# Optimization experiments

Hardware: AMD Instinct MI355X
Metric: run time of the kernel (lower is better)

## Reference

```python
import jax, jax.numpy as jnp
import numpy as np

V, SMAX, D, L, H, F = 50257, 1024, 768, 12, 12, 3072
DH = D // H
SCALE = float(np.sqrt(DH))


def setup_inputs() -> dict:
    key = jax.random.key(0)
    ks = jax.random.split(key, 24)
    B, S = 2, 1024
    std = 0.02
    inp = {
        'input_ids': jax.random.randint(ks[0], (B, S), 0, V),
        'tok_emb': jax.random.normal(ks[1], (V, D), jnp.float32) * std,
        'pos_emb': jax.random.normal(ks[2], (SMAX, D), jnp.float32) * std,
        # stacked per-layer params (leading dim L)
        'Wq': jax.random.normal(ks[3], (L, D, D), jnp.float32) * std,
        'bq': jnp.zeros((L, D), jnp.float32),
        'Wk': jax.random.normal(ks[4], (L, D, D), jnp.float32) * std,
        'bk': jnp.zeros((L, D), jnp.float32),
        'Wv': jax.random.normal(ks[5], (L, D, D), jnp.float32) * std,
        'bv': jnp.zeros((L, D), jnp.float32),
        'Wo': jax.random.normal(ks[6], (L, D, D), jnp.float32) * std,
        'bo': jnp.zeros((L, D), jnp.float32),
        'ln1_g': jnp.ones((L, D), jnp.float32),
        'ln1_b': jnp.zeros((L, D), jnp.float32),
        'ln2_g': jnp.ones((L, D), jnp.float32),
        'ln2_b': jnp.zeros((L, D), jnp.float32),
        'W1': jax.random.normal(ks[7], (L, D, F), jnp.float32) * std,
        'b1': jnp.zeros((L, F), jnp.float32),
        'W2': jax.random.normal(ks[8], (L, F, D), jnp.float32) * std,
        'b2': jnp.zeros((L, D), jnp.float32),
        'lnf_g': jnp.ones((D,), jnp.float32),
        'lnf_b': jnp.zeros((D,), jnp.float32),
        'Whead': jax.random.normal(ks[9], (D, V), jnp.float32) * std,
    }
    return inp


def _layernorm(x, g, b, eps=1e-5):
    mu = jnp.mean(x, axis=-1, keepdims=True)
    var = jnp.var(x, axis=-1, keepdims=True)
    return (x - mu) * jax.lax.rsqrt(var + eps) * g + b


def _gpt_forward(input_ids, tok_emb, pos_emb, Wq, bq, Wk, bk, Wv, bv, Wo, bo,
                 ln1_g, ln1_b, ln2_g, ln2_b, W1, b1, W2, b2, lnf_g, lnf_b, Whead):
    B, S = input_ids.shape
    x = tok_emb[input_ids] + pos_emb[:S][None, :, :]  # (B,S,D)
    # additive causal mask: -inf above the diagonal
    idx = jnp.arange(S)
    neg_inf = jnp.finfo(x.dtype).min
    mask = jnp.where(idx[None, :] > idx[:, None], neg_inf, 0.0).astype(x.dtype)  # (S,S)

    def block(x, p):
        (wq, bq_, wk, bk_, wv, bv_, wo, bo_, g1, b1_, g2, b2_, w1, bb1, w2, bb2) = p
        h = _layernorm(x, g1, b1_)
        q = (h @ wq + bq_).reshape(B, S, H, DH)
        k = (h @ wk + bk_).reshape(B, S, H, DH)
        v = (h @ wv + bv_).reshape(B, S, H, DH)
        scores = jnp.einsum('bqhd,bkhd->bhqk', q, k) / SCALE + mask
        attn = jax.nn.softmax(scores, axis=-1)
        o = jnp.einsum('bhqk,bkhd->bqhd', attn, v).reshape(B, S, D)
        x = x + (o @ wo + bo_)
        h2 = _layernorm(x, g2, b2_)
        ffn = jax.nn.gelu(h2 @ w1 + bb1, approximate=False) @ w2 + bb2
        return x + ffn, None

    params = (Wq, bq, Wk, bk, Wv, bv, Wo, bo, ln1_g, ln1_b, ln2_g, ln2_b, W1, b1, W2, b2)
    x, _ = jax.lax.scan(block, x, params)
    x = _layernorm(x, lnf_g, lnf_b)
    return x @ Whead  # (B,S,V) logits


def reference(input_ids, tok_emb, pos_emb, Wq, bq, Wk, bk, Wv, bv, Wo, bo,
              ln1_g, ln1_b, ln2_g, ln2_b, W1, b1, W2, b2, lnf_g, lnf_b, Whead):
    return _gpt_forward(input_ids, tok_emb, pos_emb, Wq, bq, Wk, bk, Wv, bv, Wo, bo,
                        ln1_g, ln1_b, ln2_g, ln2_b, W1, b1, W2, b2, lnf_g, lnf_b, Whead)
```

## Files before the change

kernel.cpp:

```cpp
#include <hip/hip_runtime.h>
#include <hip/hip_bf16.h>
#include <cstdint>
#include <cstddef>

#define DEV __device__ __forceinline__

typedef __attribute__((ext_vector_type(8))) short short8;
typedef __attribute__((ext_vector_type(4))) float f32x4;
typedef unsigned short u16;
typedef unsigned int u32;

static constexpr int Vv = 50257;
static constexpr int Dd = 768;
static constexpr int Ll = 12;
static constexpr int Hh = 12;
static constexpr int Ff = 3072;
static constexpr int Ss = 1024;
static constexpr int Bbatch = 2;
static constexpr int DHh = 64;
static constexpr int Mtok = Bbatch * Ss;
static constexpr int NQKV = 3 * Dd;
static constexpr int VPAD = 50304;

DEV float bf2f(u16 u){ u32 x = ((u32)u) << 16; float f; __builtin_memcpy(&f, &x, 4); return f; }
DEV u16 f2bf(float f){ u32 x; __builtin_memcpy(&x, &f, 4); x += 0x7fffu + ((x >> 16) & 1u); return (u16)(x >> 16); }

DEV void gld_lds16(const void* g, void* l){
  __builtin_amdgcn_global_load_lds((const __attribute__((address_space(1))) void*)g,
                                   (__attribute__((address_space(3))) void*)l, 16, 0, 0);
}

__global__ void k_embed(const int* __restrict__ ids, const float* __restrict__ tok,
                        const float* __restrict__ pos, float* __restrict__ x){
  int t = blockIdx.x;
  int id = ids[t];
  int s = t & (Ss - 1);
  const float* tr = tok + (size_t)id * Dd;
  const float* pr = pos + (size_t)s * Dd;
  float* xr = x + (size_t)t * Dd;
  for (int c = threadIdx.x; c < Dd; c += blockDim.x) xr[c] = tr[c] + pr[c];
}

__global__ __launch_bounds__(256) void k_ln(const float* __restrict__ x, const float* __restrict__ g,
                                            const float* __restrict__ b, u16* __restrict__ y){
  int row = blockIdx.x, tid = threadIdx.x;
  const float* xr = x + (size_t)row * Dd;
  float v0 = xr[tid], v1 = xr[tid + 256], v2 = xr[tid + 512];
  float s = v0 + v1 + v2, ss = v0 * v0 + v1 * v1 + v2 * v2;
  for (int o = 1; o < 64; o <<= 1){ s += __shfl_xor(s, o, 64); ss += __shfl_xor(ss, o, 64); }
  __shared__ float red[8];
  int w = tid >> 6, l = tid & 63;
  if (l == 0){ red[w] = s; red[w + 4] = ss; }
  __syncthreads();
  s = red[0] + red[1] + red[2] + red[3];
  ss = red[4] + red[5] + red[6] + red[7];
  float mu = s * (1.0f / Dd);
  float var = ss * (1.0f / Dd) - mu * mu;
  float rs = rsqrtf(var + 1e-5f);
  u16* yr = y + (size_t)row * Dd;
  yr[tid]       = f2bf((v0 - mu) * rs * g[tid]       + b[tid]);
  yr[tid + 256] = f2bf((v1 - mu) * rs * g[tid + 256] + b[tid + 256]);
  yr[tid + 512] = f2bf((v2 - mu) * rs * g[tid + 512] + b[tid + 512]);
}

__global__ void k_transpose(const float* __restrict__ src, u16* __restrict__ dst,
                            int R, int C, long smat, long dmat){
  __shared__ float tile[32][33];
  src += (size_t)blockIdx.z * smat;
  dst += (size_t)blockIdx.z * dmat;
  int c0 = blockIdx.x * 32, r0 = blockIdx.y * 32;
  int tx = threadIdx.x, ty = threadIdx.y;
  #pragma unroll
  for (int i = 0; i < 4; i++){
    int r = r0 + ty + i * 8, c = c0 + tx;
    if (c < C) tile[ty + i * 8][tx] = src[(size_t)r * C + c];
  }
  __syncthreads();
  #pragma unroll
  for (int i = 0; i < 4; i++){
    int c = c0 + ty + i * 8, r = r0 + tx;
    if (c < C) dst[(size_t)c * R + r] = f2bf(tile[tx][ty + i * 8]);
  }
}

__global__ void k_vt(const u16* __restrict__ qkv, u16* __restrict__ vt){
  __shared__ u16 tile[32][33];
  int z = blockIdx.z, b = z / Hh, h = z % Hh;
  int d0 = blockIdx.x * 32, s0 = blockIdx.y * 32;
  int tx = threadIdx.x, ty = threadIdx.y;
  #pragma unroll
  for (int i = 0; i < 4; i++){
    int sP = s0 + ty + i * 8;
    tile[ty + i * 8][tx] = qkv[(size_t)(b * Ss + sP) * NQKV + 2 * Dd + h * DHh + d0 + tx];
  }
  __syncthreads();
  #pragma unroll
  for (int i = 0; i < 4; i++){
    int d = d0 + ty + i * 8;
    vt[((size_t)(z * DHh + d)) * Ss + s0 + tx] = tile[tx][ty + i * 8];
  }
}

__global__ void k_biaspack(const float* __restrict__ bq, const float* __restrict__ bk,
                           const float* __restrict__ bv, float* __restrict__ o){
  int i = blockIdx.x * 256 + threadIdx.x;
  int col = i % NQKV, lay = i / NQKV;
  float v = (col < Dd) ? bq[lay * Dd + col]
          : (col < 2 * Dd) ? bk[lay * Dd + col - Dd]
          : bv[lay * Dd + col - 2 * Dd];
  o[i] = v;
}

template<int BM, int BN, int ACT, bool RES, bool OUTBF, bool SCALEQ, bool NB, bool HASBIAS>
__global__ __launch_bounds__(256) void k_gemm(const u16* __restrict__ A, const u16* __restrict__ Bt,
                                              const float* __restrict__ bias, const float* __restrict__ res,
                                              float* __restrict__ Cf, u16* __restrict__ Cb,
                                              int Mm, int Nn, int Kk){
  constexpr int HM = BM / 2, HN = BN / 2;
  constexpr int FM = HM / 16, FN = HN / 16;
  __shared__ __align__(16) u16 ldsA[BM * 32];
  __shared__ __align__(16) u16 ldsB[BN * 32];
  int tid = threadIdx.x, wid = tid >> 6, l = tid & 63;
  int wm = wid >> 1, wn = wid & 1;
  int m0 = blockIdx.y * BM, n0 = blockIdx.x * BN;
  int lr = l & 15, lc = l >> 4;
  f32x4 acc[FM][FN];
  #pragma unroll
  for (int i = 0; i < FM; i++)
    #pragma unroll
    for (int j = 0; j < FN; j++) acc[i][j] = (f32x4)0.0f;
  constexpr int nA = (BM * 4) / 256, nB = (BN * 4) / 256;
  for (int k0 = 0; k0 < Kk; k0 += 32){
    #pragma unroll
    for (int i = 0; i < nA; i++){
      int id = i * 256 + tid, row = id >> 2, c = id & 3;
      int cs = c ^ ((row >> 1) & 3);
      gld_lds16(A + (size_t)(m0 + row) * Kk + k0 + cs * 8,
                (char*)ldsA + (size_t)(i * 256 + (wid << 6)) * 16);
    }
    #pragma unroll
    for (int i = 0; i < nB; i++){
      int id = i * 256 + tid, row = id >> 2, c = id & 3;
      int cs = c ^ ((row >> 1) & 3);
      gld_lds16(Bt + (size_t)(n0 + row) * Kk + k0 + cs * 8,
                (char*)ldsB + (size_t)(i * 256 + (wid << 6)) * 16);
    }
    __syncthreads();
    short8 af[FM], bfr[FN];
    #pragma unroll
    for (int i = 0; i < FM; i++){
      int row = wm * HM + i * 16 + lr;
      af[i] = *(const short8*)((const char*)ldsA + row * 64 + ((lc ^ ((row >> 1) & 3)) << 4));
    }
    #pragma unroll
    for (int j = 0; j < FN; j++){
      int row = wn * HN + j * 16 + lr;
      bfr[j] = *(const short8*)((const char*)ldsB + row * 64 + ((lc ^ ((row >> 1) & 3)) << 4));
    }
    #pragma unroll
    for (int i = 0; i < FM; i++)
      #pragma unroll
      for (int j = 0; j < FN; j++)
        acc[i][j] = __builtin_amdgcn_mfma_f32_16x16x32_bf16(af[i], bfr[j], acc[i][j], 0, 0, 0);
    __syncthreads();
  }
  #pragma unroll
  for (int i = 0; i < FM; i++){
    #pragma unroll
    for (int j = 0; j < FN; j++){
      int col = n0 + wn * HN + j * 16 + lr;
      if (NB && col >= Nn) continue;
      float bv = HASBIAS ? bias[col] : 0.0f;
      #pragma unroll
      for (int r = 0; r < 4; r++){
        int row = m0 + wm * HM + i * 16 + lc * 4 + r;
        float v = acc[i][j][r] + bv;
        if (SCALEQ){ if (col < Dd) v *= 0.125f; }
        if (ACT == 1) v = 0.5f * v * (1.0f + erff(v * 0.70710678118f));
        if (RES) v += res[(size_t)row * Nn + col];
        if (OUTBF) Cb[(size_t)row * Nn + col] = f2bf(v);
        else       Cf[(size_t)row * Nn + col] = v;
      }
    }
  }
}

__global__ __launch_bounds__(256) void k_attn(const u16* __restrict__ qkv, const u16* __restrict__ vt,
                                              u16* __restrict__ o){
  __shared__ __align__(16) u16 ldsK[64 * 64];
  __shared__ __align__(16) u16 ldsV[64 * 64];
  __shared__ __align__(16) u16 ldsP[4 * 16 * 72];
  int iq = blockIdx.x, bh = blockIdx.y, b = bh / Hh, h = bh % Hh;
  int tid = threadIdx.x, wid = tid >> 6, l = tid & 63, lr = l & 15, lc = l >> 4;
  int qrow = b * Ss + iq * 64 + wid * 16 + lr;
  const u16* qp = qkv + (size_t)qrow * NQKV + h * DHh;
  short8 qf[2];
  qf[0] = *(const short8*)(qp + lc * 8);
  qf[1] = *(const short8*)(qp + 32 + lc * 8);
  float mreg[4], lsum[4];
  f32x4 oacc[4];
  #pragma unroll
  for (int r = 0; r < 4; r++){ mreg[r] = -1e30f; lsum[r] = 0.0f; }
  #pragma unroll
  for (int i = 0; i < 4; i++) oacc[i] = (f32x4)0.0f;
  u16* pbase = ldsP + wid * 16 * 72;
  for (int j = 0; j <= iq; j++){
    #pragma unroll
    for (int c = 0; c < 2; c++){
      int id = c * 256 + tid, row = id >> 3, ch = id & 7;
      int cs = ch ^ (row & 7);
      gld_lds16(qkv + (size_t)(b * Ss + j * 64 + row) * NQKV + Dd + h * DHh + cs * 8,
                (char*)ldsK + (size_t)(c * 256 + (wid << 6)) * 16);
      gld_lds16(vt + ((size_t)(bh * DHh + row)) * Ss + j * 64 + cs * 8,
                (char*)ldsV + (size_t)(c * 256 + (wid << 6)) * 16);
    }
    __syncthreads();
    f32x4 sc[4];
    #pragma unroll
    for (int fn = 0; fn < 4; fn++) sc[fn] = (f32x4)0.0f;
    #pragma unroll
    for (int fn = 0; fn < 4; fn++){
      int kv = fn * 16 + lr;
      #pragma unroll
      for (int ks = 0; ks < 2; ks++){
        int ch = ks * 4 + lc;
        short8 kf = *(const short8*)((const char*)ldsK + kv * 128 + ((ch ^ (kv & 7)) << 4));
        sc[fn] = __builtin_amdgcn_mfma_f32_16x16x32_bf16(qf[ks], kf, sc[fn], 0, 0, 0);
      }
    }
    if (j == iq){
      #pragma unroll
      for (int fn = 0; fn < 4; fn++){
        int kv = fn * 16 + lr;
        #pragma unroll
        for (int r = 0; r < 4; r++){
          int qr = wid * 16 + lc * 4 + r;
          if (kv > qr) sc[fn][r] = -1e30f;
        }
      }
    }
    float alpha[4];
    #pragma unroll
    for (int r = 0; r < 4; r++){
      float mx = fmaxf(fmaxf(sc[0][r], sc[1][r]), fmaxf(sc[2][r], sc[3][r]));
      mx = fmaxf(mx, __shfl_xor(mx, 1, 64));
      mx = fmaxf(mx, __shfl_xor(mx, 2, 64));
      mx = fmaxf(mx, __shfl_xor(mx, 4, 64));
      mx = fmaxf(mx, __shfl_xor(mx, 8, 64));
      float mnew = fmaxf(mreg[r], mx);
      alpha[r] = __expf(mreg[r] - mnew);
      mreg[r] = mnew;
      float rsum = 0.0f;
      #pragma unroll
      for (int fn = 0; fn < 4; fn++){
        float p = __expf(sc[fn][r] - mnew);
        sc[fn][r] = p;
        rsum += p;
      }
      rsum += __shfl_xor(rsum, 1, 64);
      rsum += __shfl_xor(rsum, 2, 64);
      rsum += __shfl_xor(rsum, 4, 64);
      rsum += __shfl_xor(rsum, 8, 64);
      lsum[r] = lsum[r] * alpha[r] + rsum;
    }
    #pragma unroll
    for (int fn = 0; fn < 4; fn++)
      #pragma unroll
      for (int r = 0; r < 4; r++)
        pbase[(lc * 4 + r) * 72 + fn * 16 + lr] = f2bf(sc[fn][r]);
    #pragma unroll
    for (int fd = 0; fd < 4; fd++)
      #pragma unroll
      for (int r = 0; r < 4; r++) oacc[fd][r] *= alpha[r];
    short8 pa[2];
    #pragma unroll
    for (int ks = 0; ks < 2; ks++)
      pa[ks] = *(const short8*)((const char*)pbase + lr * 144 + (ks * 4 + lc) * 16);
    #pragma unroll
    for (int fd = 0; fd < 4; fd++){
      int dd = fd * 16 + lr;
      #pragma unroll
      for (int ks = 0; ks < 2; ks++){
        int ch = ks * 4 + lc;
        short8 vf = *(const short8*)((const char*)ldsV + dd * 128 + ((ch ^ (dd & 7)) << 4));
        oacc[fd] = __builtin_amdgcn_mfma_f32_16x16x32_bf16(pa[ks], vf, oacc[fd], 0, 0, 0);
      }
    }
    __syncthreads();
  }
  #pragma unroll
  for (int fd = 0; fd < 4; fd++)
    #pragma unroll
    for (int r = 0; r < 4; r++){
      int row = b * Ss + iq * 64 + wid * 16 + lc * 4 + r;
      o[(size_t)row * Dd + h * DHh + fd * 16 + lr] = f2bf(oacc[fd][r] / lsum[r]);
    }
}

extern "C" void kernel_launch(void* const* d_in, const int* in_sizes, int n_in,
                              void* d_out, int out_size, void* d_ws, size_t ws_size,
                              hipStream_t stream){
  const int*   ids  = (const int*)d_in[0];
  const float* tok  = (const float*)d_in[1];
  const float* pos  = (const float*)d_in[2];
  const float* Wq   = (const float*)d_in[3];
  const float* bq   = (const float*)d_in[4];
  const float* Wk   = (const float*)d_in[5];
  const float* bk   = (const float*)d_in[6];
  const float* Wv   = (const float*)d_in[7];
  const float* bv   = (const float*)d_in[8];
  const float* Wo   = (const float*)d_in[9];
  const float* bo   = (const float*)d_in[10];
  const float* ln1g = (const float*)d_in[11];
  const float* ln1b = (const float*)d_in[12];
  const float* ln2g = (const float*)d_in[13];
  const float* ln2b = (const float*)d_in[14];
  const float* W1   = (const float*)d_in[15];
  const float* b1   = (const float*)d_in[16];
  const float* W2   = (const float*)d_in[17];
  const float* b2   = (const float*)d_in[18];
  const float* lnfg = (const float*)d_in[19];
  const float* lnfb = (const float*)d_in[20];
  const float* Wh   = (const float*)d_in[21];
  float* out = (float*)d_out;

  auto al = [](size_t x){ return (x + 255) & ~(size_t)255; };
  size_t off = 0;
  auto take = [&](size_t bytes){ size_t r = off; off = al(off + bytes); return r; };
  size_t o_x   = take((size_t)Mtok * Dd * 4);
  size_t o_h   = take((size_t)Mtok * Dd * 2);
  size_t o_qkv = take((size_t)Mtok * NQKV * 2);
  size_t o_vt  = take((size_t)Bbatch * Hh * DHh * Ss * 2);
  size_t o_o   = take((size_t)Mtok * Dd * 2);
  size_t o_mid = take((size_t)Mtok * Ff * 2);
  size_t o_bq  = take((size_t)Ll * NQKV * 4);
  size_t o_rot = off;
  size_t o_wqkv, o_wo, o_w1, o_w2, o_wh;
  bool full;
  {
    size_t t = off;
    o_wqkv = t; t = al(t + (size_t)Ll * NQKV * Dd * 2);
    o_wo   = t; t = al(t + (size_t)Ll * Dd * Dd * 2);
    o_w1   = t; t = al(t + (size_t)Ll * Ff * Dd * 2);
    o_w2   = t; t = al(t + (size_t)Ll * Dd * Ff * 2);
    o_wh   = t; t = al(t + (size_t)VPAD * Dd * 2);
    full = (t <= ws_size);
  }
  char* ws = (char*)d_ws;
  float* x    = (float*)(ws + o_x);
  u16*   h    = (u16*)(ws + o_h);
  u16*   qkvb = (u16*)(ws + o_qkv);
  u16*   vtb  = (u16*)(ws + o_vt);
  u16*   ob   = (u16*)(ws + o_o);
  u16*   midb = (u16*)(ws + o_mid);
  float* bqkvp= (float*)(ws + o_bq);
  u16* wqkvT = full ? (u16*)(ws + o_wqkv) : (u16*)(ws + o_rot);
  u16* woT   = full ? (u16*)(ws + o_wo)   : (u16*)(ws + o_rot);
  u16* w1T   = full ? (u16*)(ws + o_w1)   : (u16*)(ws + o_rot);
  u16* w2T   = full ? (u16*)(ws + o_w2)   : (u16*)(ws + o_rot);
  u16* whT   = full ? (u16*)(ws + o_wh)   : (u16*)(ws + o_rot);

  dim3 tb(32, 8);
  auto tpose = [&](const float* src, u16* dst, int R, int C, int nmat, long smat, long dmat){
    k_transpose<<<dim3((C + 31) / 32, R / 32, nmat), tb, 0, stream>>>(src, dst, R, C, smat, dmat);
  };

  k_biaspack<<<(Ll * NQKV) / 256, 256, 0, stream>>>(bq, bk, bv, bqkvp);
  k_embed<<<Mtok, 256, 0, stream>>>(ids, tok, pos, x);

  if (full){
    tpose(Wq, wqkvT,              Dd, Dd, Ll, (long)Dd * Dd, (long)NQKV * Dd);
    tpose(Wk, wqkvT + Dd * Dd,    Dd, Dd, Ll, (long)Dd * Dd, (long)NQKV * Dd);
    tpose(Wv, wqkvT + 2 * Dd * Dd,Dd, Dd, Ll, (long)Dd * Dd, (long)NQKV * Dd);
    tpose(Wo, woT, Dd, Dd, Ll, (long)Dd * Dd, (long)Dd * Dd);
    tpose(W1, w1T, Dd, Ff, Ll, (long)Dd * Ff, (long)Ff * Dd);
    tpose(W2, w2T, Ff, Dd, Ll, (long)Ff * Dd, (long)Dd * Ff);
    tpose(Wh, whT, Dd, Vv, 1, 0, 0);
  }

  auto gemm_qkv = [&](const u16* A, const u16* Bt, const float* bias, u16* Cb){
    k_gemm<128, 128, 0, false, true, true, false, true>
      <<<dim3(NQKV / 128, Mtok / 128), 256, 0, stream>>>(A, Bt, bias, nullptr, nullptr, Cb, Mtok, NQKV, Dd);
  };
  auto gemm_res = [&](const u16* A, const u16* Bt, const float* bias, float* C, int K){
    k_gemm<64, 128, 0, true, false, false, false, true>
      <<<dim3(Dd / 128, Mtok / 64), 256, 0, stream>>>(A, Bt, bias, C, C, nullptr, Mtok, Dd, K);
  };
  auto gemm_ffn1 = [&](const u16* A, const u16* Bt, const float* bias, u16* Cb){
    k_gemm<128, 128, 1, false, true, false, false, true>
      <<<dim3(Ff / 128, Mtok / 128), 256, 0, stream>>>(A, Bt, bias, nullptr, nullptr, Cb, Mtok, Ff, Dd);
  };
  auto gemm_head = [&](const u16* A, const u16* Bt, float* C){
    k_gemm<128, 128, 0, false, false, false, true, false>
      <<<dim3((Vv + 127) / 128, Mtok / 128), 256, 0, stream>>>(A, Bt, nullptr, nullptr, C, nullptr, Mtok, Vv, Dd);
  };

  for (int l = 0; l < Ll; ++l){
    const u16* wqkvL = full ? wqkvT + (size_t)l * NQKV * Dd : wqkvT;
    const u16* woL   = full ? woT   + (size_t)l * Dd * Dd   : woT;
    const u16* w1L   = full ? w1T   + (size_t)l * Ff * Dd   : w1T;
    const u16* w2L   = full ? w2T   + (size_t)l * Dd * Ff   : w2T;
    if (!full){
      tpose(Wq + (size_t)l * Dd * Dd, wqkvT,              Dd, Dd, 1, 0, 0);
      tpose(Wk + (size_t)l * Dd * Dd, wqkvT + Dd * Dd,    Dd, Dd, 1, 0, 0);
      tpose(Wv + (size_t)l * Dd * Dd, wqkvT + 2 * Dd * Dd,Dd, Dd, 1, 0, 0);
    }
    k_ln<<<Mtok, 256, 0, stream>>>(x, ln1g + l * Dd, ln1b + l * Dd, h);
    gemm_qkv(h, wqkvL, bqkvp + l * NQKV, qkvb);
    k_vt<<<dim3(2, 32, Bbatch * Hh), tb, 0, stream>>>(qkvb, vtb);
    k_attn<<<dim3(Ss / 64, Bbatch * Hh), 256, 0, stream>>>(qkvb, vtb, ob);
    if (!full) tpose(Wo + (size_t)l * Dd * Dd, woT, Dd, Dd, 1, 0, 0);
    gemm_res(ob, woL, bo + l * Dd, x, Dd);
    k_ln<<<Mtok, 256, 0, stream>>>(x, ln2g + l * Dd, ln2b + l * Dd, h);
    if (!full) tpose(W1 + (size_t)l * Dd * Ff, w1T, Dd, Ff, 1, 0, 0);
    gemm_ffn1(h, w1L, b1 + l * Ff, midb);
    if (!full) tpose(W2 + (size_t)l * Ff * Dd, w2T, Ff, Dd, 1, 0, 0);
    gemm_res(midb, w2L, b2 + l * Dd, x, Ff);
  }
  k_ln<<<Mtok, 256, 0, stream>>>(x, lnfg, lnfb, h);
  if (!full) tpose(Wh, whT, Dd, Vv, 1, 0, 0);
  gemm_head(h, whT, out);
}
```

Before: 2.567 ms.

## Double-buffer GEMM LDS, remap tiles across XCDs, split-K the FFN2 GEMM

The GEMM kernel now uses two LDS buffers so the next K slice is staged while the current one is computed, removing one barrier per iteration. It also switches to a 1D grid with an XCD-aware block remap. Tile sizes are shrunk for the QKV, Wo and FFN1 GEMMs to launch more workgroups. FFN2 becomes a 2-way split-K GEMM that writes fp32 partials, followed by a new combine kernel that adds the partials, bias and residual. This trades more LDS use and an extra kernel plus partial-buffer traffic for better occupancy and latency hiding.

```diff
diff --git a/kernel.cpp b/kernel.cpp
--- a/kernel.cpp
+++ b/kernel.cpp
@@ -111,58 +111,103 @@
   o[i] = v;
 }
 
-template<int BM, int BN, int ACT, bool RES, bool OUTBF, bool SCALEQ, bool NB, bool HASBIAS>
+__global__ __launch_bounds__(256) void k_combine(const float* __restrict__ p,
+                                                 const float* __restrict__ bias,
+                                                 float* __restrict__ x){
+  int i = blockIdx.x * 256 + threadIdx.x;
+  f32x4 a  = ((const f32x4*)x)[i];
+  f32x4 q0 = ((const f32x4*)p)[i];
+  f32x4 q1 = ((const f32x4*)(p + (size_t)Mtok * Dd))[i];
+  int col0 = (i * 4) % Dd;
+  f32x4 bv = *(const f32x4*)(bias + col0);
+  ((f32x4*)x)[i] = a + q0 + q1 + bv;
+}
+
+template<int BM, int BN, int ACT, bool RES, bool OUTBF, bool SCALEQ, bool NB, bool HASBIAS, bool SPLIT>
 __global__ __launch_bounds__(256) void k_gemm(const u16* __restrict__ A, const u16* __restrict__ Bt,
                                               const float* __restrict__ bias, const float* __restrict__ res,
                                               float* __restrict__ Cf, u16* __restrict__ Cb,
-                                              int Mm, int Nn, int Kk){
+                                              int Mm, int Nn, int Kk, int MT, int NT, int KS){
   constexpr int HM = BM / 2, HN = BN / 2;
   constexpr int FM = HM / 16, FN = HN / 16;
-  __shared__ __align__(16) u16 ldsA[BM * 32];
-  __shared__ __align__(16) u16 ldsB[BN * 32];
+  __shared__ __align__(16) u16 ldsA[2][BM * 32];
+  __shared__ __align__(16) u16 ldsB[2][BN * 32];
   int tid = threadIdx.x, wid = tid >> 6, l = tid & 63;
   int wm = wid >> 1, wn = wid & 1;
-  int m0 = blockIdx.y * BM, n0 = blockIdx.x * BN;
   int lr = l & 15, lc = l >> 4;
+  int nwg = gridDim.x, dIdx = blockIdx.x;
+  int L = ((nwg & 7) == 0) ? ((dIdx & 7) * (nwg >> 3) + (dIdx >> 3)) : dIdx;
+  int kidx = 0;
+  if (SPLIT){ int per = MT * NT; kidx = L / per; L -= kidx * per; }
+  int mtile = L % MT, ntile = L / MT;
+  int m0 = mtile * BM, n0 = ntile * BN;
+  int klen = Kk / KS, kbase = kidx * klen, nk = klen >> 5;
+
   f32x4 acc[FM][FN];
   #pragma unroll
   for (int i = 0; i < FM; i++)
     #pragma unroll
     for (int j = 0; j < FN; j++) acc[i][j] = (f32x4)0.0f;
+
   constexpr int nA = (BM * 4) / 256, nB = (BN * 4) / 256;
-  for (int k0 = 0; k0 < Kk; k0 += 32){
+  auto stage = [&](int buf, int kk){
     #pragma unroll
     for (int i = 0; i < nA; i++){
       int id = i * 256 + tid, row = id >> 2, c = id & 3;
       int cs = c ^ ((row >> 1) & 3);
-      gld_lds16(A + (size_t)(m0 + row) * Kk + k0 + cs * 8,
-                (char*)ldsA + (size_t)(i * 256 + (wid << 6)) * 16);
+      gld_lds16(A + (size_t)(m0 + row) * Kk + kk + cs * 8,
+                (char*)ldsA[buf] + (size_t)(i * 256 + (wid << 6)) * 16);
     }
     #pragma unroll
     for (int i = 0; i < nB; i++){
       int id = i * 256 + tid, row = id >> 2, c = id & 3;
       int cs = c ^ ((row >> 1) & 3);
-      gld_lds16(Bt + (size_t)(n0 + row) * Kk + k0 + cs * 8,
-                (char*)ldsB + (size_t)(i * 256 + (wid << 6)) * 16);
-    }
-    __syncthreads();
+      gld_lds16(Bt + (size_t)(n0 + row) * Kk + kk + cs * 8,
+                (char*)ldsB[buf] + (size_t)(i * 256 + (wid << 6)) * 16);
+    }
+  };
+  auto compute = [&](int buf){
     short8 af[FM], bfr[FN];
     #pragma unroll
     for (int i = 0; i < FM; i++){
       int row = wm * HM + i * 16 + lr;
-      af[i] = *(const short8*)((const char*)ldsA + row * 64 + ((lc ^ ((row >> 1) & 3)) << 4));
+      af[i] = *(const short8*)((const char*)ldsA[buf] + row * 64 + ((lc ^ ((row >> 1) & 3)) << 4));
     }
     #pragma unroll
     for (int j = 0; j < FN; j++){
       int row = wn * HN + j * 16 + lr;
-      bfr[j] = *(const short8*)((const char*)ldsB + row * 64 + ((lc ^ ((row >> 1) & 3)) << 4));
+      bfr[j] = *(const short8*)((const char*)ldsB[buf] + row * 64 + ((lc ^ ((row >> 1) & 3)) << 4));
     }
     #pragma unroll
     for (int i = 0; i < FM; i++)
       #pragma unroll
       for (int j = 0; j < FN; j++)
         acc[i][j] = __builtin_amdgcn_mfma_f32_16x16x32_bf16(af[i], bfr[j], acc[i][j], 0, 0, 0);
+  };
+
+  stage(0, kbase);
+  __syncthreads();
+  for (int t = 0; t < nk - 1; ++t){
+    stage((t + 1) & 1, kbase + (t + 1) * 32);
+    compute(t & 1);
     __syncthreads();
+  }
+  compute((nk - 1) & 1);
+
+  if (SPLIT){
+    float* P = Cf + (size_t)kidx * Mm * Nn;
+    #pragma unroll
+    for (int i = 0; i < FM; i++)
+      #pragma unroll
+      for (int j = 0; j < FN; j++){
+        int col = n0 + wn * HN + j * 16 + lr;
+        #pragma unroll
+        for (int r = 0; r < 4; r++){
+          int row = m0 + wm * HM + i * 16 + lc * 4 + r;
+          P[(size_t)row * Nn + col] = acc[i][j][r];
+        }
+      }
+    return;
   }
   #pragma unroll
   for (int i = 0; i < FM; i++){
@@ -327,13 +372,14 @@
   auto al = [](size_t x){ return (x + 255) & ~(size_t)255; };
   size_t off = 0;
   auto take = [&](size_t bytes){ size_t r = off; off = al(off + bytes); return r; };
-  size_t o_x   = take((size_t)Mtok * Dd * 4);
-  size_t o_h   = take((size_t)Mtok * Dd * 2);
-  size_t o_qkv = take((size_t)Mtok * NQKV * 2);
-  size_t o_vt  = take((size_t)Bbatch * Hh * DHh * Ss * 2);
-  size_t o_o   = take((size_t)Mtok * Dd * 2);
-  size_t o_mid = take((size_t)Mtok * Ff * 2);
-  size_t o_bq  = take((size_t)Ll * NQKV * 4);
+  size_t o_x    = take((size_t)Mtok * Dd * 4);
+  size_t o_h    = take((size_t)Mtok * Dd * 2);
+  size_t o_qkv  = take((size_t)Mtok * NQKV * 2);
+  size_t o_vt   = take((size_t)Bbatch * Hh * DHh * Ss * 2);
+  size_t o_o    = take((size_t)Mtok * Dd * 2);
+  size_t o_mid  = take((size_t)Mtok * Ff * 2);
+  size_t o_bq   = take((size_t)Ll * NQKV * 4);
+  size_t o_part = take((size_t)2 * Mtok * Dd * 4);
   size_t o_rot = off;
   size_t o_wqkv, o_wo, o_w1, o_w2, o_wh;
   bool full;
@@ -354,6 +400,7 @@
   u16*   ob   = (u16*)(ws + o_o);
   u16*   midb = (u16*)(ws + o_mid);
   float* bqkvp= (float*)(ws + o_bq);
+  float* part = (float*)(ws + o_part);
   u16* wqkvT = full ? (u16*)(ws + o_wqkv) : (u16*)(ws + o_rot);
   u16* woT   = full ? (u16*)(ws + o_wo)   : (u16*)(ws + o_rot);
   u16* w1T   = full ? (u16*)(ws + o_w1)   : (u16*)(ws + o_rot);
@@ -379,20 +426,29 @@
   }
 
   auto gemm_qkv = [&](const u16* A, const u16* Bt, const float* bias, u16* Cb){
-    k_gemm<128, 128, 0, false, true, true, false, true>
-      <<<dim3(NQKV / 128, Mtok / 128), 256, 0, stream>>>(A, Bt, bias, nullptr, nullptr, Cb, Mtok, NQKV, Dd);
-  };
-  auto gemm_res = [&](const u16* A, const u16* Bt, const float* bias, float* C, int K){
-    k_gemm<64, 128, 0, true, false, false, false, true>
-      <<<dim3(Dd / 128, Mtok / 64), 256, 0, stream>>>(A, Bt, bias, C, C, nullptr, Mtok, Dd, K);
+    constexpr int MT = Mtok / 64, NT = NQKV / 128;
+    k_gemm<64, 128, 0, false, true, true, false, true, false>
+      <<<MT * NT, 256, 0, stream>>>(A, Bt, bias, nullptr, nullptr, Cb, Mtok, NQKV, Dd, MT, NT, 1);
+  };
+  auto gemm_wo = [&](const u16* A, const u16* Bt, const float* bias, float* C){
+    constexpr int MT = Mtok / 64, NT = Dd / 64;
+    k_gemm<64, 64, 0, true, false, false, false, true, false>
+      <<<MT * NT, 256, 0, stream>>>(A, Bt, bias, C, C, nullptr, Mtok, Dd, Dd, MT, NT, 1);
   };
   auto gemm_ffn1 = [&](const u16* A, const u16* Bt, const float* bias, u16* Cb){
-    k_gemm<128, 128, 1, false, true, false, false, true>
-      <<<dim3(Ff / 128, Mtok / 128), 256, 0, stream>>>(A, Bt, bias, nullptr, nullptr, Cb, Mtok, Ff, Dd);
+    constexpr int MT = Mtok / 64, NT = Ff / 128;
+    k_gemm<64, 128, 1, false, true, false, false, true, false>
+      <<<MT * NT, 256, 0, stream>>>(A, Bt, bias, nullptr, nullptr, Cb, Mtok, Ff, Dd, MT, NT, 1);
+  };
+  auto gemm_ffn2 = [&](const u16* A, const u16* Bt){
+    constexpr int MT = Mtok / 64, NT = Dd / 64;
+    k_gemm<64, 64, 0, false, false, false, false, false, true>
+      <<<MT * NT * 2, 256, 0, stream>>>(A, Bt, nullptr, nullptr, part, nullptr, Mtok, Dd, Ff, MT, NT, 2);
   };
   auto gemm_head = [&](const u16* A, const u16* Bt, float* C){
-    k_gemm<128, 128, 0, false, false, false, true, false>
-      <<<dim3((Vv + 127) / 128, Mtok / 128), 256, 0, stream>>>(A, Bt, nullptr, nullptr, C, nullptr, Mtok, Vv, Dd);
+    constexpr int MT = Mtok / 128, NT = VPAD / 128;
+    k_gemm<128, 128, 0, false, false, false, true, false, false>
+      <<<MT * NT, 256, 0, stream>>>(A, Bt, nullptr, nullptr, C, nullptr, Mtok, Vv, Dd, MT, NT, 1);
   };
 
   for (int l = 0; l < Ll; ++l){
@@ -410,12 +466,13 @@
     k_vt<<<dim3(2, 32, Bbatch * Hh), tb, 0, stream>>>(qkvb, vtb);
     k_attn<<<dim3(Ss / 64, Bbatch * Hh), 256, 0, stream>>>(qkvb, vtb, ob);
     if (!full) tpose(Wo + (size_t)l * Dd * Dd, woT, Dd, Dd, 1, 0, 0);
-    gemm_res(ob, woL, bo + l * Dd, x, Dd);
+    gemm_wo(ob, woL, bo + l * Dd, x);
     k_ln<<<Mtok, 256, 0, stream>>>(x, ln2g + l * Dd, ln2b + l * Dd, h);
     if (!full) tpose(W1 + (size_t)l * Dd * Ff, w1T, Dd, Ff, 1, 0, 0);
     gemm_ffn1(h, w1L, b1 + l * Ff, midb);
     if (!full) tpose(W2 + (size_t)l * Ff * Dd, w2T, Ff, Dd, 1, 0, 0);
-    gemm_res(midb, w2L, b2 + l * Dd, x, Ff);
+    gemm_ffn2(midb, w2L);
+    k_combine<<<(Mtok * Dd / 4) / 256, 256, 0, stream>>>(part, b2 + l * Dd, x);
   }
   k_ln<<<Mtok, 256, 0, stream>>>(x, lnfg, lnfb, h);
   if (!full) tpose(Wh, whT, Dd, Vv, 1, 0, 0);
```

New measurement: 2.235 ms. 12.9% less time.
